# Optimization experiments

Hardware: AMD Instinct MI355X
Metric: run time of the kernel (lower is better)

Reference implementation:

```python
import jax, jax.numpy as jnp
import numpy as np
import math

ALPHA = 1.0
LAMBDA1 = 0.5
DELTA = 1.0
SIGMA = 1.0
SPACING = 2.0
N_UNITS = 8
M_ATOMS = 1024


def setup_inputs() -> dict:
    key = jax.random.key(0)
    k1, k2, k3 = jax.random.split(key, 3)
    # positions initialized on a circle of radius SPACING with small z noise (as in __init__)
    ang = 2.0 * math.pi / N_UNITS
    i = np.arange(N_UNITS)
    pos = np.stack([SPACING * np.cos(i * ang), SPACING * np.sin(i * ang), np.zeros(N_UNITS)], axis=1).astype(np.float32)
    positions = jnp.asarray(pos) + 0.1 * jax.random.normal(k1, (N_UNITS, 3), jnp.float32) * jnp.array([0.0, 0.0, 1.0], jnp.float32)
    euler_angles = jax.random.normal(k2, (N_UNITS, 3), jnp.float32)
    coordinates = jax.random.normal(k3, (M_ATOMS, 3), jnp.float32)
    return {"positions": positions, "euler_angles": euler_angles, "coordinates": coordinates}


def _rotation_matrices(euler):  # [n,3] -> [n,3,3], R = Rz @ Ry @ Rx
    phi, theta, psi = euler[:, 0], euler[:, 1], euler[:, 2]
    cp, sp = jnp.cos(phi), jnp.sin(phi)
    ct, st = jnp.cos(theta), jnp.sin(theta)
    cs, ss = jnp.cos(psi), jnp.sin(psi)
    z = jnp.zeros_like(phi)
    o = jnp.ones_like(phi)
    Rz = jnp.stack([jnp.stack([cs, -ss, z], -1), jnp.stack([ss, cs, z], -1), jnp.stack([z, z, o], -1)], -2)
    Ry = jnp.stack([jnp.stack([ct, z, st], -1), jnp.stack([z, o, z], -1), jnp.stack([-st, z, ct], -1)], -2)
    Rx = jnp.stack([jnp.stack([o, z, z], -1), jnp.stack([z, cp, -sp], -1), jnp.stack([z, sp, cp], -1)], -2)
    return Rz @ Ry @ Rx


def reference(positions, euler_angles, coordinates):
    n = positions.shape[0]
    m = coordinates.shape[0]
    R = _rotation_matrices(euler_angles)  # [n,3,3]
    # transformed[i, x] = R_i @ coords[x] + positions[i]   -> [n, m, 3]
    transformed = jnp.einsum('nij,mj->nmi', R, coordinates) + positions[:, None, :]
    L1 = jnp.mean(jnp.sum(transformed ** 2, axis=(1, 2)))
    com = jnp.sum(positions, axis=0)
    L_com = ALPHA * jnp.sum(com ** 2)
    # interaction: sum over unit pairs i<j, all atom pairs (x1,x2) of exp(-(d2 - delta^2)/sigma^2)
    pts = transformed.reshape(n * m, 3)  # N = n*m points
    sq = jnp.sum(pts ** 2, axis=1)
    d2 = sq[:, None] + sq[None, :] - 2.0 * (pts @ pts.T)  # [N, N]
    pen = jnp.exp(-(d2 - DELTA ** 2) / (SIGMA ** 2))
    unit = jnp.arange(n * m) // m
    mask = unit[:, None] < unit[None, :]  # only cross-unit pairs, i < j
    L_int = LAMBDA1 * jnp.sum(jnp.where(mask, pen, 0.0))
    return L1 + L_com + L_int
```

## Files before the change

kernel.cpp:

```cpp
#include <hip/hip_runtime.h>

#define N_UNITS 8
#define M_ATOMS 1024
#define NP (N_UNITS * M_ATOMS)


__global__ __launch_bounds__(256) void prep_kernel(
    const float* __restrict__ pos, const float* __restrict__ euler,
    const float* __restrict__ coords, float4* __restrict__ pts,
    double* __restrict__ accum) {
  const int i = blockIdx.x * 256 + threadIdx.x;
  const int u = i >> 10;
  const int k = i & 1023;
  const float phi = euler[u * 3 + 0];
  const float theta = euler[u * 3 + 1];
  const float psi = euler[u * 3 + 2];
  const float cp = cosf(phi), sp = sinf(phi);
  const float ct = cosf(theta), st = sinf(theta);
  const float cs = cosf(psi), ss = sinf(psi);
  const float R00 = cs * ct, R01 = cs * st * sp - ss * cp, R02 = cs * st * cp + ss * sp;
  const float R10 = ss * ct, R11 = ss * st * sp + cs * cp, R12 = ss * st * cp - cs * sp;
  const float R20 = -st,     R21 = ct * sp,                R22 = ct * cp;
  const float cx = coords[k * 3 + 0];
  const float cy = coords[k * 3 + 1];
  const float cz = coords[k * 3 + 2];
  const float x = R00 * cx + R01 * cy + R02 * cz + pos[u * 3 + 0];
  const float y = R10 * cx + R11 * cy + R12 * cz + pos[u * 3 + 1];
  const float z = R20 * cx + R21 * cy + R22 * cz + pos[u * 3 + 2];
  pts[i] = make_float4(x, y, z, 0.0f);

  float sq = x * x + y * y + z * z;
  for (int off = 32; off > 0; off >>= 1) sq += __shfl_down(sq, off);
  __shared__ float wsum[4];
  if ((threadIdx.x & 63) == 0) wsum[threadIdx.x >> 6] = sq;
  __syncthreads();
  if (threadIdx.x == 0)
    atomicAdd(&accum[0], (double)(wsum[0] + wsum[1] + wsum[2] + wsum[3]));
}

__global__ __launch_bounds__(256) void pair_kernel(
    const float4* __restrict__ pts, double* __restrict__ accum) {
  int bp = blockIdx.x >> 4;
  const int t = blockIdx.x & 15;
  const int ti = t >> 2, tj = t & 3;
  int a = 0, cnt = N_UNITS - 1;
  while (bp >= cnt) { bp -= cnt; a++; cnt--; }
  const int b = a + 1 + bp;

  __shared__ float4 sh[256];
  const int i = a * M_ATOMS + ti * 256 + threadIdx.x;
  const float4 p = pts[i];
  const int j0 = b * M_ATOMS + tj * 256;
  sh[threadIdx.x] = pts[j0 + threadIdx.x];
  __syncthreads();

  float acc = 0.0f;
#pragma unroll 8
  for (int jj = 0; jj < 256; ++jj) {
    const float4 q = sh[jj];
    const float dx = p.x - q.x;
    const float dy = p.y - q.y;
    const float dz = p.z - q.z;
    const float d2 = dx * dx + dy * dy + dz * dz;
    acc += __expf(1.0f - d2);
  }
  for (int off = 32; off > 0; off >>= 1) acc += __shfl_down(acc, off);
  __shared__ float wsum[4];
  if ((threadIdx.x & 63) == 0) wsum[threadIdx.x >> 6] = acc;
  __syncthreads();
  if (threadIdx.x == 0)
    atomicAdd(&accum[1], (double)(wsum[0] + wsum[1] + wsum[2] + wsum[3]));
}

__global__ void final_kernel(const float* __restrict__ pos,
                             const double* __restrict__ accum,
                             float* __restrict__ out) {
  double cx = 0.0, cy = 0.0, cz = 0.0;
  for (int u = 0; u < N_UNITS; ++u) {
    cx += (double)pos[u * 3 + 0];
    cy += (double)pos[u * 3 + 1];
    cz += (double)pos[u * 3 + 2];
  }
  const double L1 = accum[0] / (double)N_UNITS;
  const double Lcom = cx * cx + cy * cy + cz * cz;
  const double Lint = 0.5 * accum[1];
  out[0] = (float)(L1 + Lcom + Lint);
}

extern "C" void kernel_launch(void* const* d_in, const int* in_sizes, int n_in,
                              void* d_out, int out_size, void* d_ws, size_t ws_size,
                              hipStream_t stream) {
  const float* pos = (const float*)d_in[0];
  const float* euler = (const float*)d_in[1];
  const float* coords = (const float*)d_in[2];
  double* accum = (double*)d_ws;
  float4* pts = (float4*)((char*)d_ws + 256);

  hipMemsetAsync(d_ws, 0, 256, stream);
  prep_kernel<<<NP / 256, 256, 0, stream>>>(pos, euler, coords, pts, accum);
  pair_kernel<<<28 * 16, 256, 0, stream>>>(pts, accum);
  final_kernel<<<1, 1, 0, stream>>>(pos, accum, (float*)d_out);
}
```

Measured before the change: 75.49 us.

## Fuse point transform into pair kernel and factor exp into dot-product form

```diff
diff --git a/kernel.cpp b/kernel.cpp
--- a/kernel.cpp
+++ b/kernel.cpp
@@ -2,89 +2,125 @@
 
 #define N_UNITS 8
 #define M_ATOMS 1024
-#define NP (N_UNITS * M_ATOMS)
+#define LOG2E 1.44269504088896340736f
 
-
-__global__ __launch_bounds__(256) void prep_kernel(
-    const float* __restrict__ pos, const float* __restrict__ euler,
-    const float* __restrict__ coords, float4* __restrict__ pts,
-    double* __restrict__ accum) {
-  const int i = blockIdx.x * 256 + threadIdx.x;
-  const int u = i >> 10;
-  const int k = i & 1023;
+__device__ __forceinline__ void unit_transform(const float* __restrict__ euler,
+                                               const float* __restrict__ pos,
+                                               int u, float R[9], float t[3]) {
   const float phi = euler[u * 3 + 0];
   const float theta = euler[u * 3 + 1];
   const float psi = euler[u * 3 + 2];
-  const float cp = cosf(phi), sp = sinf(phi);
-  const float ct = cosf(theta), st = sinf(theta);
-  const float cs = cosf(psi), ss = sinf(psi);
-  const float R00 = cs * ct, R01 = cs * st * sp - ss * cp, R02 = cs * st * cp + ss * sp;
-  const float R10 = ss * ct, R11 = ss * st * sp + cs * cp, R12 = ss * st * cp - cs * sp;
-  const float R20 = -st,     R21 = ct * sp,                R22 = ct * cp;
-  const float cx = coords[k * 3 + 0];
-  const float cy = coords[k * 3 + 1];
-  const float cz = coords[k * 3 + 2];
-  const float x = R00 * cx + R01 * cy + R02 * cz + pos[u * 3 + 0];
-  const float y = R10 * cx + R11 * cy + R12 * cz + pos[u * 3 + 1];
-  const float z = R20 * cx + R21 * cy + R22 * cz + pos[u * 3 + 2];
-  pts[i] = make_float4(x, y, z, 0.0f);
-
-  float sq = x * x + y * y + z * z;
-  for (int off = 32; off > 0; off >>= 1) sq += __shfl_down(sq, off);
-  __shared__ float wsum[4];
-  if ((threadIdx.x & 63) == 0) wsum[threadIdx.x >> 6] = sq;
-  __syncthreads();
-  if (threadIdx.x == 0)
-    atomicAdd(&accum[0], (double)(wsum[0] + wsum[1] + wsum[2] + wsum[3]));
+  const float cp = __cosf(phi), sp = __sinf(phi);
+  const float ct = __cosf(theta), st = __sinf(theta);
+  const float cs = __cosf(psi), sn = __sinf(psi);
+  R[0] = cs * ct; R[1] = cs * st * sp - sn * cp; R[2] = cs * st * cp + sn * sp;
+  R[3] = sn * ct; R[4] = sn * st * sp + cs * cp; R[5] = sn * st * cp - cs * sp;
+  R[6] = -st;     R[7] = ct * sp;                R[8] = ct * cp;
+  t[0] = pos[u * 3 + 0]; t[1] = pos[u * 3 + 1]; t[2] = pos[u * 3 + 2];
 }
 
-__global__ __launch_bounds__(256) void pair_kernel(
-    const float4* __restrict__ pts, double* __restrict__ accum) {
+__global__ __launch_bounds__(256) void fused_kernel(
+    const float* __restrict__ pos, const float* __restrict__ euler,
+    const float* __restrict__ coords, float2* __restrict__ out) {
   int bp = blockIdx.x >> 4;
-  const int t = blockIdx.x & 15;
-  const int ti = t >> 2, tj = t & 3;
+  const int jt = blockIdx.x & 15;
   int a = 0, cnt = N_UNITS - 1;
   while (bp >= cnt) { bp -= cnt; a++; cnt--; }
   const int b = a + 1 + bp;
+  const int tid = threadIdx.x;
 
-  __shared__ float4 sh[256];
-  const int i = a * M_ATOMS + ti * 256 + threadIdx.x;
-  const float4 p = pts[i];
-  const int j0 = b * M_ATOMS + tj * 256;
-  sh[threadIdx.x] = pts[j0 + threadIdx.x];
+  float Ra[9], ta[3], Rb[9], tb[3];
+  unit_transform(euler, pos, a, Ra, ta);
+  unit_transform(euler, pos, b, Rb, tb);
+
+  __shared__ float4 sh[64];
+  float jqq = 0.0f;
+  if (tid < 64) {
+    const int k = jt * 64 + tid;
+    const float cx = coords[k * 3 + 0];
+    const float cy = coords[k * 3 + 1];
+    const float cz = coords[k * 3 + 2];
+    const float qx = Rb[0] * cx + Rb[1] * cy + Rb[2] * cz + tb[0];
+    const float qy = Rb[3] * cx + Rb[4] * cy + Rb[5] * cz + tb[1];
+    const float qz = Rb[6] * cx + Rb[7] * cy + Rb[8] * cz + tb[2];
+    jqq = qx * qx + qy * qy + qz * qz;
+    sh[tid] = make_float4(2.0f * LOG2E * qx, 2.0f * LOG2E * qy,
+                          2.0f * LOG2E * qz, -LOG2E * jqq);
+  }
+
+  float px[4], py[4], pz[4], A[4];
+  float ipp = 0.0f;
+#pragma unroll
+  for (int k = 0; k < 4; ++k) {
+    const int i = k * 256 + tid;
+    const float cx = coords[i * 3 + 0];
+    const float cy = coords[i * 3 + 1];
+    const float cz = coords[i * 3 + 2];
+    const float x = Ra[0] * cx + Ra[1] * cy + Ra[2] * cz + ta[0];
+    const float y = Ra[3] * cx + Ra[4] * cy + Ra[5] * cz + ta[1];
+    const float z = Ra[6] * cx + Ra[7] * cy + Ra[8] * cz + ta[2];
+    px[k] = x; py[k] = y; pz[k] = z;
+    const float pp = x * x + y * y + z * z;
+    ipp += pp;
+    A[k] = LOG2E - LOG2E * pp;
+  }
   __syncthreads();
 
-  float acc = 0.0f;
+  float acc0 = 0.0f, acc1 = 0.0f, acc2 = 0.0f, acc3 = 0.0f;
 #pragma unroll 8
-  for (int jj = 0; jj < 256; ++jj) {
+  for (int jj = 0; jj < 64; ++jj) {
     const float4 q = sh[jj];
-    const float dx = p.x - q.x;
-    const float dy = p.y - q.y;
-    const float dz = p.z - q.z;
-    const float d2 = dx * dx + dy * dy + dz * dz;
-    acc += __expf(1.0f - d2);
+    acc0 += __builtin_amdgcn_exp2f(fmaf(px[0], q.x, fmaf(py[0], q.y, fmaf(pz[0], q.z, q.w))));
+    acc1 += __builtin_amdgcn_exp2f(fmaf(px[1], q.x, fmaf(py[1], q.y, fmaf(pz[1], q.z, q.w))));
+    acc2 += __builtin_amdgcn_exp2f(fmaf(px[2], q.x, fmaf(py[2], q.y, fmaf(pz[2], q.z, q.w))));
+    acc3 += __builtin_amdgcn_exp2f(fmaf(px[3], q.x, fmaf(py[3], q.y, fmaf(pz[3], q.z, q.w))));
   }
-  for (int off = 32; off > 0; off >>= 1) acc += __shfl_down(acc, off);
-  __shared__ float wsum[4];
-  if ((threadIdx.x & 63) == 0) wsum[threadIdx.x >> 6] = acc;
+  float part = __builtin_amdgcn_exp2f(A[0]) * acc0 +
+               __builtin_amdgcn_exp2f(A[1]) * acc1 +
+               __builtin_amdgcn_exp2f(A[2]) * acc2 +
+               __builtin_amdgcn_exp2f(A[3]) * acc3;
+
+  float ssq = 0.0f;
+  if (a == 0) ssq += jqq;
+  if (blockIdx.x == 0) ssq += ipp;
+
+  for (int off = 32; off > 0; off >>= 1) {
+    part += __shfl_down(part, off);
+    ssq += __shfl_down(ssq, off);
+  }
+  __shared__ float redp[4], reds[4];
+  if ((tid & 63) == 0) { redp[tid >> 6] = part; reds[tid >> 6] = ssq; }
   __syncthreads();
-  if (threadIdx.x == 0)
-    atomicAdd(&accum[1], (double)(wsum[0] + wsum[1] + wsum[2] + wsum[3]));
+  if (tid == 0)
+    out[blockIdx.x] = make_float2(redp[0] + redp[1] + redp[2] + redp[3],
+                                  reds[0] + reds[1] + reds[2] + reds[3]);
 }
 
-__global__ void final_kernel(const float* __restrict__ pos,
-                             const double* __restrict__ accum,
-                             float* __restrict__ out) {
-  double cx = 0.0, cy = 0.0, cz = 0.0;
-  for (int u = 0; u < N_UNITS; ++u) {
-    cx += (double)pos[u * 3 + 0];
-    cy += (double)pos[u * 3 + 1];
-    cz += (double)pos[u * 3 + 2];
+__global__ __launch_bounds__(64) void final_kernel(
+    const float* __restrict__ pos, const float2* __restrict__ partials,
+    float* __restrict__ outp) {
+  const int tid = threadIdx.x;
+  float pairS = 0.0f, ssS = 0.0f;
+  for (int idx = tid; idx < 28 * 16; idx += 64) {
+    const float2 v = partials[idx];
+    pairS += v.x;
+    ssS += v.y;
   }
-  const double L1 = accum[0] / (double)N_UNITS;
-  const double Lcom = cx * cx + cy * cy + cz * cz;
-  const double Lint = 0.5 * accum[1];
-  out[0] = (float)(L1 + Lcom + Lint);
+  for (int off = 32; off > 0; off >>= 1) {
+    pairS += __shfl_down(pairS, off);
+    ssS += __shfl_down(ssS, off);
+  }
+  if (tid == 0) {
+    float cx = 0.0f, cy = 0.0f, cz = 0.0f;
+    for (int u = 0; u < N_UNITS; ++u) {
+      cx += pos[u * 3 + 0];
+      cy += pos[u * 3 + 1];
+      cz += pos[u * 3 + 2];
+    }
+    const float L1 = ssS * (1.0f / N_UNITS);
+    const float Lcom = cx * cx + cy * cy + cz * cz;
+    outp[0] = L1 + Lcom + 0.5f * pairS;
+  }
 }
 
 extern "C" void kernel_launch(void* const* d_in, const int* in_sizes, int n_in,
@@ -93,11 +129,8 @@
   const float* pos = (const float*)d_in[0];
   const float* euler = (const float*)d_in[1];
   const float* coords = (const float*)d_in[2];
-  double* accum = (double*)d_ws;
-  float4* pts = (float4*)((char*)d_ws + 256);
+  float2* partials = (float2*)d_ws;
 
-  hipMemsetAsync(d_ws, 0, 256, stream);
-  prep_kernel<<<NP / 256, 256, 0, stream>>>(pos, euler, coords, pts, accum);
-  pair_kernel<<<28 * 16, 256, 0, stream>>>(pts, accum);
-  final_kernel<<<1, 1, 0, stream>>>(pos, accum, (float*)d_out);
+  fused_kernel<<<28 * 16, 256, 0, stream>>>(pos, euler, coords, partials);
+  final_kernel<<<1, 64, 0, stream>>>(pos, partials, (float*)d_out);
 }
```

Result: faster. 65.95 us (-12.6%).
